# Optimization experiments

Measured on AMD Instinct MI355X. Metric: run time of the kernel, lower is better.

## Reference

```python
import jax, jax.numpy as jnp
import numpy as np

N, E, G = 40000, 640000, 64
D_IN, D_EMB, D_HID, D_OUT = 128, 128, 128, 36


def setup_inputs() -> dict:
    key = jax.random.key(0)
    ks = jax.random.split(key, 12)
    x = jax.random.normal(ks[0], (N, D_IN), dtype=jnp.float32)
    edge_weight = jax.random.uniform(ks[1], (E,), dtype=jnp.float32)
    rho = jax.random.uniform(ks[2], (G,), dtype=jnp.float32)
    edge_index = jax.random.randint(ks[3], (2, E), 0, N, dtype=jnp.int32)
    batch = jnp.sort(jax.random.randint(ks[4], (N,), 0, G, dtype=jnp.int32))
    def lin(k, fi, fo):
        s = 1.0 / np.sqrt(fi)
        return jax.random.normal(k, (fi, fo), dtype=jnp.float32) * s
    conv_w = lin(ks[5], D_IN, D_EMB)
    conv_b = jnp.zeros((D_EMB,), jnp.float32)
    w1 = lin(ks[6], 2 * D_EMB + 1, D_HID); b1 = jnp.zeros((D_HID,), jnp.float32)
    w2 = lin(ks[7], D_HID, D_HID);        b2 = jnp.zeros((D_HID,), jnp.float32)
    w3 = lin(ks[8], D_HID, D_OUT);        b3 = jnp.zeros((D_OUT,), jnp.float32)
    return dict(x=x, edge_weight=edge_weight, rho=rho, conv_w=conv_w, conv_b=conv_b,
                w1=w1, b1=b1, w2=w2, b2=b2, w3=w3, b3=b3,
                edge_index=edge_index, batch=batch)


def _gcn_conv(h, edge_index, ew, W, b):
    # PyG GCNConv: add self-loops (weight 1), symmetric deg^-1/2 normalization,
    # linear transform, gather-scale-scatter aggregation, bias.
    n = h.shape[0]
    loop = jnp.arange(n, dtype=edge_index.dtype)
    src = jnp.concatenate([edge_index[0], loop])
    dst = jnp.concatenate([edge_index[1], loop])
    w_all = jnp.concatenate([ew, jnp.ones((n,), ew.dtype)])
    deg = jax.ops.segment_sum(w_all, dst, num_segments=n)
    dinv = jnp.where(deg > 0, jax.lax.rsqrt(deg), 0.0)
    norm = dinv[src] * w_all * dinv[dst]          # [E+N]
    hW = h @ W                                    # [N, D_EMB]
    msg = hW[src] * norm[:, None]                 # [E+N, D_EMB]
    return jax.ops.segment_sum(msg, dst, num_segments=n) + b


def reference(x, edge_weight, rho, conv_w, conv_b, w1, b1, w2, b2, w3, b3,
              edge_index, batch):
    h = jax.nn.relu(_gcn_conv(x, edge_index, edge_weight, conv_w, conv_b))
    g = G
    cnt = jax.ops.segment_sum(jnp.ones((h.shape[0],), h.dtype), batch, num_segments=g)
    hmax = jax.ops.segment_max(h, batch, num_segments=g)
    hmax = jnp.where(cnt[:, None] > 0, hmax, 0.0)
    hsum = jax.ops.segment_sum(h, batch, num_segments=g)
    hmean = hsum / jnp.maximum(cnt, 1.0)[:, None]
    hg = jnp.concatenate([hmax, hmean, rho[:, None]], axis=1)  # [G, 2*D_EMB+1]
    z = jax.nn.relu(hg @ w1 + b1)
    z = jax.nn.relu(z @ w2 + b2)
    return z @ w3 + b3
```

## Files before the change

kernel.cpp:

```cpp
#include <hip/hip_runtime.h>
#include <hip/hip_bf16.h>
#include <hip/hip_fp16.h>

static __device__ __forceinline__ float relu_f(float v) { return v > 0.f ? v : 0.f; }

typedef _Float16 half8 __attribute__((ext_vector_type(8)));
typedef float floatx4 __attribute__((ext_vector_type(4)));

#define ELL 96

static __device__ __forceinline__ float entry_w(unsigned int pk) {
  return __half2float(__ushort_as_half((unsigned short)(pk >> 16)));
}


__global__ void cast_init_kernel(const float4* __restrict__ x4, __half2* __restrict__ xh2,
                                 int n4, int* __restrict__ indeg, int n,
                                 float* __restrict__ gmax, float* __restrict__ gsum,
                                 float* __restrict__ gcnt, int gch, int g,
                                 const float* __restrict__ W, _Float16* __restrict__ wt) {
  int i = blockIdx.x * blockDim.x + threadIdx.x;
  if (i < n4) {
    float4 v = x4[i];
    xh2[2 * i + 0] = __floats2half2_rn(v.x, v.y);
    xh2[2 * i + 1] = __floats2half2_rn(v.z, v.w);
  }
  if (i < n) indeg[i] = 0;
  if (i < gch) { gmax[i] = 0.f; gsum[i] = 0.f; }
  if (i < g) gcnt[i] = 0.f;
  if (i < 128 * 128) {
    int k = i >> 7, nn = i & 127;
    wt[nn * 128 + k] = (_Float16)W[i];
  }
}


__global__ void count_fill_kernel(const int* __restrict__ src, const int* __restrict__ dst,
                                  const float* __restrict__ ew, int* __restrict__ indeg,
                                  unsigned int* __restrict__ epack, int E) {
  int e = blockIdx.x * blockDim.x + threadIdx.x;
  if (e >= E) return;
  int d = dst[e];
  int r = atomicAdd(&indeg[d], 1);
  if (r < ELL) {
    unsigned short w16 = __half_as_ushort(__float2half_rn(ew[e]));
    epack[(size_t)d * ELL + r] = (unsigned int)src[e] | ((unsigned int)w16 << 16);
  }
}

__global__ void row_dinv_kernel(const int* __restrict__ indeg, unsigned int* __restrict__ epack,
                                float* __restrict__ dinv, int n) {
  int i = blockIdx.x * blockDim.x + threadIdx.x;
  if (i >= n) return;
  size_t s = (size_t)i * ELL;
  int deg = indeg[i];
  size_t re = s + deg;
  size_t e = s + ((deg + 7) & ~7);
  float d = 1.0f;
  for (size_t j = s; j < re; ++j) d += entry_w(epack[j]);
  for (size_t j = re; j < e; ++j) epack[j] = 0u;
  dinv[i] = (d > 0.f) ? rsqrtf(d) : 0.f;
}


__global__ __launch_bounds__(256) void agg_gemm_pool_kernel(const half8* __restrict__ xh8,
    const float* __restrict__ dinv, const int* __restrict__ indeg,
    const unsigned int* __restrict__ epack, const _Float16* __restrict__ wt,
    const float* __restrict__ bias, const int* __restrict__ batch,
    float* __restrict__ gmax, float* __restrict__ gsum, float* __restrict__ gcnt, int n) {
  __shared__ float sH[64 * 129];
  _Float16* sAgg = (_Float16*)sH;
  __shared__ int sBatch[64];
  int tid = threadIdx.x;
  int w = tid >> 6, lane = tid & 63;
  int grp = lane >> 4, sub = lane & 15;
  int quad = lane >> 4, c15 = lane & 15;
  int row0 = blockIdx.x * 64;
  int nb = n - row0; if (nb > 64) nb = 64;

  #pragma unroll
  for (int it = 0; it < 4; ++it) {
    int rloc = w * 16 + it * 4 + grp;
    int node = row0 + rloc;
    if (node >= n) node = n - 1;
    float dn = dinv[node];
    half8 xv = xh8[(size_t)node * 16 + sub];
    float sw = dn * dn;
    float acc[8];
    #pragma unroll
    for (int c = 0; c < 8; ++c) acc[c] = sw * (float)xv[c];
    size_t base = (size_t)node * ELL;
    int dlen = (indeg[node] + 7) & ~7;
    for (int j = 0; j < dlen; j += 8) {
      uint4 pa = *(const uint4*)&epack[base + j];
      uint4 pb = *(const uint4*)&epack[base + j + 4];
      unsigned int pk[8] = {pa.x, pa.y, pa.z, pa.w, pb.x, pb.y, pb.z, pb.w};
      half8 hx[8];
      float dw[8];
      #pragma unroll
      for (int u = 0; u < 8; ++u) {
        int sidx = (int)(pk[u] & 0xFFFFu);
        hx[u] = xh8[(size_t)sidx * 16 + sub];
        dw[u] = dinv[sidx];
      }
      #pragma unroll
      for (int u = 0; u < 8; ++u) {
        float wgt = dw[u] * entry_w(pk[u]) * dn;
        #pragma unroll
        for (int c = 0; c < 8; ++c) acc[c] += wgt * (float)hx[u][c];
      }
    }
    half8 outv;
    #pragma unroll
    for (int c = 0; c < 8; ++c) outv[c] = (_Float16)acc[c];
    *(half8*)&sAgg[rloc * 136 + sub * 8] = outv;
  }
  __syncthreads();

  half8 af[4];
  #pragma unroll
  for (int ks = 0; ks < 4; ++ks)
    af[ks] = *(const half8*)&sAgg[(w * 16 + c15) * 136 + ks * 32 + quad * 8];
  if (tid < nb) sBatch[tid] = batch[row0 + tid];
  __syncthreads();

  float bb[8];
  #pragma unroll
  for (int j = 0; j < 8; ++j) bb[j] = bias[j * 16 + c15];

  floatx4 acc[8] = {};
  #pragma unroll
  for (int ks = 0; ks < 4; ++ks) {
    #pragma unroll
    for (int j = 0; j < 8; ++j) {
      const half8* bptr =
          (const half8*)(wt + (size_t)(j * 16 + c15) * 128 + ks * 32 + quad * 8);
      acc[j] = __builtin_amdgcn_mfma_f32_16x16x32_f16(af[ks], *bptr, acc[j], 0, 0, 0);
    }
  }

  #pragma unroll
  for (int j = 0; j < 8; ++j) {
    int col = j * 16 + c15;
    #pragma unroll
    for (int r = 0; r < 4; ++r) {
      int row = w * 16 + quad * 4 + r;
      if (row < nb) sH[row * 129 + col] = relu_f(acc[j][r] + bb[j]);
    }
  }
  __syncthreads();

  if (tid < 128) {
    int c = tid;
    int cur = sBatch[0];
    float mx = 0.f, sm = 0.f;
    int cnt = 0;
    for (int r = 0; r < nb; ++r) {
      int g = sBatch[r];
      if (g != cur) {
        atomicMax((int*)&gmax[cur * 128 + c], __float_as_int(mx));
        atomicAdd(&gsum[cur * 128 + c], sm);
        if (c == 0) atomicAdd(&gcnt[cur], (float)cnt);
        mx = 0.f; sm = 0.f; cnt = 0; cur = g;
      }
      float v = sH[r * 129 + c];
      mx = fmaxf(mx, v);
      sm += v;
      ++cnt;
    }
    atomicMax((int*)&gmax[cur * 128 + c], __float_as_int(mx));
    atomicAdd(&gsum[cur * 128 + c], sm);
    if (c == 0) atomicAdd(&gcnt[cur], (float)cnt);
  }
}


__global__ __launch_bounds__(128) void mlp_kernel(const float* __restrict__ gmax,
    const float* __restrict__ gsum, const float* __restrict__ gcnt,
    const float* __restrict__ rho,
    const float* __restrict__ w1, const float* __restrict__ b1,
    const float* __restrict__ w2, const float* __restrict__ b2,
    const float* __restrict__ w3, const float* __restrict__ b3,
    float* __restrict__ out) {
  __shared__ float s_in[257];
  __shared__ float s_z1[128];
  __shared__ float s_z2[128];
  int g = blockIdx.x, t = threadIdx.x;
  float inv_cnt = 1.f / fmaxf(gcnt[g], 1.f);
  s_in[t] = gmax[g * 128 + t];
  s_in[128 + t] = gsum[g * 128 + t] * inv_cnt;
  if (t == 0) s_in[256] = rho[g];
  __syncthreads();
  float s = b1[t];
  for (int k = 0; k < 257; ++k) s += s_in[k] * w1[k * 128 + t];
  s_z1[t] = relu_f(s);
  __syncthreads();
  s = b2[t];
  for (int k = 0; k < 128; ++k) s += s_z1[k] * w2[k * 128 + t];
  s_z2[t] = relu_f(s);
  __syncthreads();
  if (t < 36) {
    s = b3[t];
    for (int k = 0; k < 128; ++k) s += s_z2[k] * w3[k * 36 + t];
    out[g * 36 + t] = s;
  }
}


extern "C" void kernel_launch(void* const* d_in, const int* in_sizes, int n_in,
                              void* d_out, int out_size, void* d_ws, size_t ws_size,
                              hipStream_t stream) {
  const float* x      = (const float*)d_in[0];
  const float* ew     = (const float*)d_in[1];
  const float* rho    = (const float*)d_in[2];
  const float* conv_w = (const float*)d_in[3];
  const float* conv_b = (const float*)d_in[4];
  const float* w1 = (const float*)d_in[5];
  const float* b1 = (const float*)d_in[6];
  const float* w2 = (const float*)d_in[7];
  const float* b2 = (const float*)d_in[8];
  const float* w3 = (const float*)d_in[9];
  const float* b3 = (const float*)d_in[10];
  const int* eidx  = (const int*)d_in[11];
  const int* batch = (const int*)d_in[12];

  const int N = in_sizes[0] / 128;
  const int E = in_sizes[1];
  const int G = in_sizes[2];
  const int* srcp = eidx;
  const int* dstp = eidx + E;

  char* p = (char*)d_ws;
  auto carve = [&](size_t bytes) { char* r = p; p += (bytes + 255) & ~(size_t)255; return (void*)r; };
  float*        dinv  = (float*)       carve((size_t)N * 4);
  int*          indeg = (int*)         carve((size_t)N * 4);
  unsigned int* epack = (unsigned int*)carve((size_t)N * ELL * 4);
  __half2*      xh    = (__half2*)     carve((size_t)N * 128 * 2);
  _Float16*     wt    = (_Float16*)    carve((size_t)128 * 128 * 2);
  float*        gmax  = (float*)       carve((size_t)G * 128 * 4);
  float*        gsum  = (float*)       carve((size_t)G * 128 * 4);
  float*        gcnt  = (float*)       carve((size_t)G * 4);

  const int n4 = N * 32;

  cast_init_kernel<<<(n4 + 255) / 256, 256, 0, stream>>>((const float4*)x, xh, n4,
                                                         indeg, N, gmax, gsum, gcnt,
                                                         G * 128, G, conv_w, wt);
  count_fill_kernel<<<(E + 255) / 256, 256, 0, stream>>>(srcp, dstp, ew, indeg, epack, E);
  row_dinv_kernel<<<(N + 255) / 256, 256, 0, stream>>>(indeg, epack, dinv, N);
  agg_gemm_pool_kernel<<<(N + 63) / 64, 256, 0, stream>>>((const half8*)xh, dinv, indeg,
                                                          epack, wt, conv_b, batch,
                                                          gmax, gsum, gcnt, N);
  mlp_kernel<<<G, 128, 0, stream>>>(gmax, gsum, gcnt, rho, w1, b1, w2, b2, w3, b3,
                                    (float*)d_out);
}
```

Before: 193.6 us.

## Fuse degree accumulation into packed 64-bit atomic and pre-scale features by dinv

The edge count and the fixed-point weighted degree are accumulated together in one 64-bit atomic per edge, which removes the separate row_dinv pass over the ELL rows. Source features are pre-multiplied by their own deg^-1/2 during the fp16 cast, so the aggregation loop no longer gathers dinv per neighbour. Padding entries are masked inside the loop instead of being zeroed in memory. The cost is a fixed-point weight sum with 24 fractional bits, which limits accuracy on the summed degree, and extra select instructions in the inner loop.

```diff
diff --git a/kernel.cpp b/kernel.cpp
--- a/kernel.cpp
+++ b/kernel.cpp
@@ -1,5 +1,4 @@
 #include <hip/hip_runtime.h>
-#include <hip/hip_bf16.h>
 #include <hip/hip_fp16.h>
 
 static __device__ __forceinline__ float relu_f(float v) { return v > 0.f ? v : 0.f; }
@@ -14,18 +13,12 @@
 }
 
 
-__global__ void cast_init_kernel(const float4* __restrict__ x4, __half2* __restrict__ xh2,
-                                 int n4, int* __restrict__ indeg, int n,
-                                 float* __restrict__ gmax, float* __restrict__ gsum,
-                                 float* __restrict__ gcnt, int gch, int g,
-                                 const float* __restrict__ W, _Float16* __restrict__ wt) {
+__global__ void init_kernel(unsigned long long* __restrict__ cnt, int n,
+                            float* __restrict__ gmax, float* __restrict__ gsum,
+                            float* __restrict__ gcnt, int gch, int g,
+                            const float* __restrict__ W, _Float16* __restrict__ wt) {
   int i = blockIdx.x * blockDim.x + threadIdx.x;
-  if (i < n4) {
-    float4 v = x4[i];
-    xh2[2 * i + 0] = __floats2half2_rn(v.x, v.y);
-    xh2[2 * i + 1] = __floats2half2_rn(v.z, v.w);
-  }
-  if (i < n) indeg[i] = 0;
+  if (i < n) cnt[i] = 0ull;
   if (i < gch) { gmax[i] = 0.f; gsum[i] = 0.f; }
   if (i < g) gcnt[i] = 0.f;
   if (i < 128 * 128) {
@@ -36,35 +29,44 @@
 
 
 __global__ void count_fill_kernel(const int* __restrict__ src, const int* __restrict__ dst,
-                                  const float* __restrict__ ew, int* __restrict__ indeg,
+                                  const float* __restrict__ ew,
+                                  unsigned long long* __restrict__ cnt,
                                   unsigned int* __restrict__ epack, int E) {
   int e = blockIdx.x * blockDim.x + threadIdx.x;
   if (e >= E) return;
   int d = dst[e];
-  int r = atomicAdd(&indeg[d], 1);
+  float w = ew[e];
+  unsigned long long pk = (1ull << 32) | (unsigned long long)__float2uint_rn(w * 16777216.f);
+  unsigned long long old = atomicAdd(&cnt[d], pk);
+  unsigned int r = (unsigned int)(old >> 32);
   if (r < ELL) {
-    unsigned short w16 = __half_as_ushort(__float2half_rn(ew[e]));
+    unsigned short w16 = __half_as_ushort(__float2half_rn(w));
     epack[(size_t)d * ELL + r] = (unsigned int)src[e] | ((unsigned int)w16 << 16);
   }
 }
 
-__global__ void row_dinv_kernel(const int* __restrict__ indeg, unsigned int* __restrict__ epack,
-                                float* __restrict__ dinv, int n) {
-  int i = blockIdx.x * blockDim.x + threadIdx.x;
-  if (i >= n) return;
-  size_t s = (size_t)i * ELL;
-  int deg = indeg[i];
-  size_t re = s + deg;
-  size_t e = s + ((deg + 7) & ~7);
-  float d = 1.0f;
-  for (size_t j = s; j < re; ++j) d += entry_w(epack[j]);
-  for (size_t j = re; j < e; ++j) epack[j] = 0u;
-  dinv[i] = (d > 0.f) ? rsqrtf(d) : 0.f;
+
+__global__ void premul_cast_kernel(const float4* __restrict__ x4,
+                                   const unsigned long long* __restrict__ cnt,
+                                   half8* __restrict__ xh8, int n) {
+  int j = blockIdx.x * blockDim.x + threadIdx.x;
+  if (j >= n * 16) return;
+  int node = j >> 4;
+  unsigned long long cv = cnt[node];
+  float deg = 1.f + (float)(unsigned int)cv * (1.f / 16777216.f);
+  float dinv = rsqrtf(deg);
+  float4 a = x4[2 * j], b = x4[2 * j + 1];
+  half8 o;
+  o[0] = (_Float16)(a.x * dinv); o[1] = (_Float16)(a.y * dinv);
+  o[2] = (_Float16)(a.z * dinv); o[3] = (_Float16)(a.w * dinv);
+  o[4] = (_Float16)(b.x * dinv); o[5] = (_Float16)(b.y * dinv);
+  o[6] = (_Float16)(b.z * dinv); o[7] = (_Float16)(b.w * dinv);
+  xh8[j] = o;
 }
 
 
 __global__ __launch_bounds__(256) void agg_gemm_pool_kernel(const half8* __restrict__ xh8,
-    const float* __restrict__ dinv, const int* __restrict__ indeg,
+    const unsigned long long* __restrict__ cnt,
     const unsigned int* __restrict__ epack, const _Float16* __restrict__ wt,
     const float* __restrict__ bias, const int* __restrict__ batch,
     float* __restrict__ gmax, float* __restrict__ gsum, float* __restrict__ gcnt, int n) {
@@ -83,29 +85,29 @@
     int rloc = w * 16 + it * 4 + grp;
     int node = row0 + rloc;
     if (node >= n) node = n - 1;
-    float dn = dinv[node];
+    unsigned long long cv = cnt[node];
+    int deg = (int)(unsigned int)(cv >> 32);
+    if (deg > ELL) deg = ELL;
+    float dn = rsqrtf(1.f + (float)(unsigned int)cv * (1.f / 16777216.f));
     half8 xv = xh8[(size_t)node * 16 + sub];
-    float sw = dn * dn;
     float acc[8];
     #pragma unroll
-    for (int c = 0; c < 8; ++c) acc[c] = sw * (float)xv[c];
+    for (int c = 0; c < 8; ++c) acc[c] = dn * (float)xv[c];
     size_t base = (size_t)node * ELL;
-    int dlen = (indeg[node] + 7) & ~7;
+    int dlen = (deg + 7) & ~7;
     for (int j = 0; j < dlen; j += 8) {
       uint4 pa = *(const uint4*)&epack[base + j];
       uint4 pb = *(const uint4*)&epack[base + j + 4];
       unsigned int pk[8] = {pa.x, pa.y, pa.z, pa.w, pb.x, pb.y, pb.z, pb.w};
       half8 hx[8];
-      float dw[8];
       #pragma unroll
       for (int u = 0; u < 8; ++u) {
-        int sidx = (int)(pk[u] & 0xFFFFu);
+        int sidx = (j + u < deg) ? (int)(pk[u] & 0xFFFFu) : node;
         hx[u] = xh8[(size_t)sidx * 16 + sub];
-        dw[u] = dinv[sidx];
       }
       #pragma unroll
       for (int u = 0; u < 8; ++u) {
-        float wgt = dw[u] * entry_w(pk[u]) * dn;
+        float wgt = (j + u < deg) ? entry_w(pk[u]) * dn : 0.f;
         #pragma unroll
         for (int c = 0; c < 8; ++c) acc[c] += wgt * (float)hx[u][c];
       }
@@ -154,23 +156,23 @@
     int c = tid;
     int cur = sBatch[0];
     float mx = 0.f, sm = 0.f;
-    int cnt = 0;
+    int cnt_ = 0;
     for (int r = 0; r < nb; ++r) {
       int g = sBatch[r];
       if (g != cur) {
         atomicMax((int*)&gmax[cur * 128 + c], __float_as_int(mx));
         atomicAdd(&gsum[cur * 128 + c], sm);
-        if (c == 0) atomicAdd(&gcnt[cur], (float)cnt);
-        mx = 0.f; sm = 0.f; cnt = 0; cur = g;
+        if (c == 0) atomicAdd(&gcnt[cur], (float)cnt_);
+        mx = 0.f; sm = 0.f; cnt_ = 0; cur = g;
       }
       float v = sH[r * 129 + c];
       mx = fmaxf(mx, v);
       sm += v;
-      ++cnt;
+      ++cnt_;
     }
     atomicMax((int*)&gmax[cur * 128 + c], __float_as_int(mx));
     atomicAdd(&gsum[cur * 128 + c], sm);
-    if (c == 0) atomicAdd(&gcnt[cur], (float)cnt);
+    if (c == 0) atomicAdd(&gcnt[cur], (float)cnt_);
   }
 }
 
@@ -232,25 +234,24 @@
 
   char* p = (char*)d_ws;
   auto carve = [&](size_t bytes) { char* r = p; p += (bytes + 255) & ~(size_t)255; return (void*)r; };
-  float*        dinv  = (float*)       carve((size_t)N * 4);
-  int*          indeg = (int*)         carve((size_t)N * 4);
-  unsigned int* epack = (unsigned int*)carve((size_t)N * ELL * 4);
-  __half2*      xh    = (__half2*)     carve((size_t)N * 128 * 2);
-  _Float16*     wt    = (_Float16*)    carve((size_t)128 * 128 * 2);
-  float*        gmax  = (float*)       carve((size_t)G * 128 * 4);
-  float*        gsum  = (float*)       carve((size_t)G * 128 * 4);
-  float*        gcnt  = (float*)       carve((size_t)G * 4);
-
-  const int n4 = N * 32;
-
-  cast_init_kernel<<<(n4 + 255) / 256, 256, 0, stream>>>((const float4*)x, xh, n4,
-                                                         indeg, N, gmax, gsum, gcnt,
-                                                         G * 128, G, conv_w, wt);
-  count_fill_kernel<<<(E + 255) / 256, 256, 0, stream>>>(srcp, dstp, ew, indeg, epack, E);
-  row_dinv_kernel<<<(N + 255) / 256, 256, 0, stream>>>(indeg, epack, dinv, N);
-  agg_gemm_pool_kernel<<<(N + 63) / 64, 256, 0, stream>>>((const half8*)xh, dinv, indeg,
-                                                          epack, wt, conv_b, batch,
-                                                          gmax, gsum, gcnt, N);
+  unsigned long long* cnt  = (unsigned long long*)carve((size_t)N * 8);
+  unsigned int*       epack = (unsigned int*)     carve((size_t)N * ELL * 4);
+  half8*              xh    = (half8*)            carve((size_t)N * 128 * 2);
+  _Float16*           wt    = (_Float16*)         carve((size_t)128 * 128 * 2);
+  float*              gmax  = (float*)            carve((size_t)G * 128 * 4);
+  float*              gsum  = (float*)            carve((size_t)G * 128 * 4);
+  float*              gcnt  = (float*)            carve((size_t)G * 4);
+
+  int m = N;
+  if (G * 128 > m) m = G * 128;
+  if (128 * 128 > m) m = 128 * 128;
+
+  init_kernel<<<(m + 255) / 256, 256, 0, stream>>>(cnt, N, gmax, gsum, gcnt,
+                                                   G * 128, G, conv_w, wt);
+  count_fill_kernel<<<(E + 255) / 256, 256, 0, stream>>>(srcp, dstp, ew, cnt, epack, E);
+  premul_cast_kernel<<<(N * 16 + 255) / 256, 256, 0, stream>>>((const float4*)x, cnt, xh, N);
+  agg_gemm_pool_kernel<<<(N + 63) / 64, 256, 0, stream>>>(xh, cnt, epack, wt, conv_b,
+                                                          batch, gmax, gsum, gcnt, N);
   mlp_kernel<<<G, 128, 0, stream>>>(gmax, gsum, gcnt, rho, w1, b1, w2, b2, w3, b3,
                                     (float*)d_out);
 }
```

New measurement: 190.9 us. About the same (-1.4%).
